# Optimization experiments

Measured on AMD Instinct MI355X. Metric: run time of the kernel, lower is better.

The kernel has to match this reference:

```python
import jax, jax.numpy as jnp
import numpy as np

B, S, H, I, L, NH = 1, 256, 384, 1536, 2, 8

def _gelu(x):
    return jax.nn.gelu(x, approximate=False)  # torch nn.GELU default = exact erf

def _ln(x, g, b, eps=1e-5):
    m = x.mean(-1, keepdims=True)
    v = jnp.var(x, axis=-1, keepdims=True)
    return (x - m) / jnp.sqrt(v + eps) * g + b

def _mha(x, Wqkv, bqkv, Wo, bo):
    b_, s_, h_ = x.shape
    d = h_ // NH
    qkv = x @ Wqkv.T + bqkv  # [B,S,3H]
    q, k, v = jnp.split(qkv, 3, axis=-1)
    sp = lambda t: t.reshape(b_, s_, NH, d).transpose(0, 2, 1, 3)  # [B,NH,S,d]
    q, k, v = sp(q), sp(k), sp(v)
    att = jax.nn.softmax(jnp.einsum('bhqd,bhkd->bhqk', q * (1.0 / np.sqrt(d)), k), axis=-1)
    o = jnp.einsum('bhqk,bhkd->bhqd', att, v).transpose(0, 2, 1, 3).reshape(b_, s_, h_)
    return o @ Wo.T + bo

def _forward(hidden_states, Wqkv, bqkv, Wo, bo, W1, b1, W2, b2, g1, be1, g2, be2,
             Wbil, bbil, Wc1, bc1, Wc2, bc2, Wih, bih, Whh, bhh, Wp1, bp1, Wp2, bp2,
             Wout, bout, reasoning_steps):
    x = hidden_states
    rstate = jnp.zeros((x.shape[0], x.shape[-1]), x.dtype)
    cprobs, conts = [], []
    for _ in range(reasoning_steps):
        # symbolic reasoning layers (eval mode: dropout off)
        for l in range(L):
            x = _ln(x + _mha(x, Wqkv[l], bqkv[l], Wo[l], bo[l]), g1[l], be1[l])
            ff = _gelu(x @ W1[l].T + b1[l]) @ W2[l].T + b2[l]
            x = _ln(x + ff, g2[l], be2[l])
        # contradiction detector: bilinear over all token pairs
        tmp = jnp.einsum('bix,oxy->bioy', x, Wbil)            # [B,S,H,H]
        inter = jnp.einsum('bioy,bjy->bijo', tmp, x) + bbil   # [B,S,S,H]
        h1 = _gelu(inter @ Wc1.T + bc1)                       # [B,S,S,H]
        logits = jnp.einsum('bijh,h->bij', h1, Wc2[0]) + bc2[0]
        cprobs.append(jax.nn.sigmoid(logits))
        # recursive reasoning controller (GRUCell on mean-pooled states)
        pooled = x.mean(axis=1)
        gi = pooled @ Wih.T + bih
        gh = rstate @ Whh.T + bhh
        ir, iz, inn = jnp.split(gi, 3, axis=-1)
        hr, hz, hn = jnp.split(gh, 3, axis=-1)
        r = jax.nn.sigmoid(ir + hr)
        z = jax.nn.sigmoid(iz + hz)
        n = jnp.tanh(inn + r * hn)
        rstate = (1.0 - z) * n + z * rstate
        conts.append(jax.nn.sigmoid(_gelu(rstate @ Wp1.T + bp1) @ Wp2[0] + bp2[0]))
    final = x @ Wout.T + bout
    return final, jnp.stack(cprobs), jnp.stack(conts)

def setup_inputs():
    key = jax.random.key(0)
    ks = iter(jax.random.split(key, 40))
    rn = lambda shape, s=0.02: jax.random.normal(next(ks), shape, jnp.float32) * s
    return {
        'hidden_states': jax.random.normal(next(ks), (B, S, H), jnp.float32),
        'Wqkv': rn((L, 3 * H, H)), 'bqkv': jnp.zeros((L, 3 * H)),
        'Wo': rn((L, H, H)), 'bo': jnp.zeros((L, H)),
        'W1': rn((L, I, H)), 'b1': jnp.zeros((L, I)),
        'W2': rn((L, H, I)), 'b2': jnp.zeros((L, H)),
        'g1': jnp.ones((L, H)), 'be1': jnp.zeros((L, H)),
        'g2': jnp.ones((L, H)), 'be2': jnp.zeros((L, H)),
        'Wbil': rn((H, H, H)), 'bbil': jnp.zeros((H,)),
        'Wc1': rn((H, H)), 'bc1': jnp.zeros((H,)),
        'Wc2': rn((1, H)), 'bc2': jnp.zeros((1,)),
        'Wih': rn((3 * H, H)), 'bih': jnp.zeros((3 * H,)),
        'Whh': rn((3 * H, H)), 'bhh': jnp.zeros((3 * H,)),
        'Wp1': rn((H, H)), 'bp1': jnp.zeros((H,)),
        'Wp2': rn((1, H)), 'bp2': jnp.zeros((1,)),
        'Wout': rn((H, H)), 'bout': jnp.zeros((H,)),
        'reasoning_steps': 2,
    }

def reference(hidden_states, Wqkv, bqkv, Wo, bo, W1, b1, W2, b2, g1, be1, g2, be2,
              Wbil, bbil, Wc1, bc1, Wc2, bc2, Wih, bih, Whh, bhh, Wp1, bp1, Wp2, bp2,
              Wout, bout, reasoning_steps):
    return _forward(hidden_states, Wqkv, bqkv, Wo, bo, W1, b1, W2, b2, g1, be1, g2, be2,
                    Wbil, bbil, Wc1, bc1, Wc2, bc2, Wih, bih, Whh, bhh, Wp1, bp1, Wp2, bp2,
                    Wout, bout, reasoning_steps)
```

## Files before the change

### kernel.cpp

```cpp
#include <hip/hip_runtime.h>

typedef __attribute__((ext_vector_type(4))) float f32x4;
typedef __attribute__((ext_vector_type(8))) short s16x8;

#define DEVI __device__ __forceinline__

DEVI float b2f(short s) {
  union { float f; unsigned u; } v; v.u = ((unsigned)(unsigned short)s) << 16; return v.f;
}
DEVI short f2b(float f) {
  union { float f; unsigned u; } v; v.f = f;
  unsigned u = v.u;
  u += 0x7FFFu + ((u >> 16) & 1u);
  return (short)(u >> 16);
}
DEVI float gelu_f(float x) {
  float z2 = 1.5957691216f * x * (1.0f + 0.044715f * x * x);
  float e = __expf(z2);
  float th = 1.0f - 2.0f / (e + 1.0f);
  return 0.5f * x * (1.0f + th);
}
DEVI float sigm_f(float x) { return 1.0f / (1.0f + expf(-x)); }

DEVI void gld16(const short* g, const short* l) {
  __builtin_amdgcn_global_load_lds((const __attribute__((address_space(1))) void*)g,
                                   (__attribute__((address_space(3))) void*)l, 16, 0, 0);
}

template<bool BIAS, bool GELU_ACT, bool OUT_BF16>
__global__ __launch_bounds__(256)
void gemm_fast_k(const short* __restrict__ A, const short* __restrict__ B,
                 const float* __restrict__ bias, void* __restrict__ Cv,
                 int M, int N, int K,
                 long long sA, long long sB, long long sC)
{
  __shared__ short As[128 * 64];
  __shared__ short Bs[128 * 64];
  const int bz = blockIdx.z;
  const int n0 = blockIdx.x * 128;
  const int m0 = blockIdx.y * 128;
  const int t = threadIdx.x, lane = t & 63, wave = t >> 6;
  const int wm = wave >> 1, wn = wave & 1;
  const short* Ab = A + bz * sA;
  const short* Bb = B + bz * sB;
  const int srow = lane >> 3;
  const int scol = ((lane & 7) ^ srow) * 8;
  const int fr = lane & 15, fs = lane >> 4;

  f32x4 acc[4][4];
#pragma unroll
  for (int i = 0; i < 4; ++i)
#pragma unroll
    for (int j = 0; j < 4; ++j) acc[i][j] = f32x4{0.f, 0.f, 0.f, 0.f};

  for (int k0 = 0; k0 < K; k0 += 64) {
#pragma unroll
    for (int q = 0; q < 4; ++q) {
      int c = wave * 4 + q;
      gld16(Ab + (long long)(m0 + c * 8 + srow) * K + k0 + scol, &As[c * 512]);
      gld16(Bb + (long long)(n0 + c * 8 + srow) * K + k0 + scol, &Bs[c * 512]);
    }
    __syncthreads();
    s16x8 af[4][2], bfv[4][2];
#pragma unroll
    for (int i = 0; i < 4; ++i) {
      int row = wm * 64 + i * 16 + fr;
#pragma unroll
      for (int s = 0; s < 2; ++s)
        af[i][s] = *(const s16x8*)&As[row * 64 + (((s * 4 + fs) ^ (fr & 7)) * 8)];
    }
#pragma unroll
    for (int j = 0; j < 4; ++j) {
      int row = wn * 64 + j * 16 + fr;
#pragma unroll
      for (int s = 0; s < 2; ++s)
        bfv[j][s] = *(const s16x8*)&Bs[row * 64 + (((s * 4 + fs) ^ (fr & 7)) * 8)];
    }
#pragma unroll
    for (int s = 0; s < 2; ++s)
#pragma unroll
      for (int i = 0; i < 4; ++i)
#pragma unroll
        for (int j = 0; j < 4; ++j)
          acc[i][j] = __builtin_amdgcn_mfma_f32_16x16x32_bf16(af[i][s], bfv[j][s], acc[i][j], 0, 0, 0);
    __syncthreads();
  }

#pragma unroll
  for (int i = 0; i < 4; ++i) {
    int rowb = m0 + wm * 64 + i * 16 + fs * 4;
#pragma unroll
    for (int j = 0; j < 4; ++j) {
      int col = n0 + wn * 64 + j * 16 + fr;
      float bb = BIAS ? bias[col] : 0.0f;
#pragma unroll
      for (int u = 0; u < 4; ++u) {
        float v = acc[i][j][u] + bb;
        if constexpr (GELU_ACT) v = gelu_f(v);
        long long off = bz * sC + (long long)(rowb + u) * N + col;
        if constexpr (OUT_BF16) ((short*)Cv)[off] = f2b(v);
        else                    ((float*)Cv)[off] = v;
      }
    }
  }
}

template<bool BIAS, bool GELU_ACT, bool OUT_BF16>
__global__ __launch_bounds__(256)
void gemm64_k(const short* __restrict__ A, const short* __restrict__ B,
              const float* __restrict__ bias, void* __restrict__ Cv,
              int M, int N, int K)
{
  __shared__ short As[64 * 32];
  __shared__ short Bs[64 * 32];
  const int n0 = blockIdx.x * 64;
  const int m0 = blockIdx.y * 64;
  const int t = threadIdx.x, lane = t & 63, wave = t >> 6;
  const int wm = wave >> 1, wn = wave & 1;
  const int srow = lane >> 2;
  const int scol = (lane & 3) * 8;
  const int fr = lane & 15, fs = lane >> 4;

  f32x4 acc[2][2];
#pragma unroll
  for (int i = 0; i < 2; ++i)
#pragma unroll
    for (int j = 0; j < 2; ++j) acc[i][j] = f32x4{0.f, 0.f, 0.f, 0.f};

  for (int k0 = 0; k0 < K; k0 += 32) {
    gld16(A + (long long)(m0 + wave * 16 + srow) * K + k0 + scol, &As[wave * 512]);
    gld16(B + (long long)(n0 + wave * 16 + srow) * K + k0 + scol, &Bs[wave * 512]);
    __syncthreads();
    s16x8 af[2], bfv[2];
#pragma unroll
    for (int i = 0; i < 2; ++i) af[i]  = *(const s16x8*)&As[(wm * 32 + i * 16 + fr) * 32 + fs * 8];
#pragma unroll
    for (int j = 0; j < 2; ++j) bfv[j] = *(const s16x8*)&Bs[(wn * 32 + j * 16 + fr) * 32 + fs * 8];
#pragma unroll
    for (int i = 0; i < 2; ++i)
#pragma unroll
      for (int j = 0; j < 2; ++j)
        acc[i][j] = __builtin_amdgcn_mfma_f32_16x16x32_bf16(af[i], bfv[j], acc[i][j], 0, 0, 0);
    __syncthreads();
  }

#pragma unroll
  for (int i = 0; i < 2; ++i) {
    int rowb = m0 + wm * 32 + i * 16 + fs * 4;
#pragma unroll
    for (int j = 0; j < 2; ++j) {
      int col = n0 + wn * 32 + j * 16 + fr;
      float bb = BIAS ? bias[col] : 0.0f;
#pragma unroll
      for (int u = 0; u < 4; ++u) {
        float v = acc[i][j][u] + bb;
        if constexpr (GELU_ACT) v = gelu_f(v);
        long long off = (long long)(rowb + u) * N + col;
        if constexpr (OUT_BF16) ((short*)Cv)[off] = f2b(v);
        else                    ((float*)Cv)[off] = v;
      }
    }
  }
}

__global__ __launch_bounds__(256)
void transpose_k(const float* __restrict__ W, short* __restrict__ WT)
{
  __shared__ short L[64 * 68];
  const int o  = blockIdx.z;
  const int x0 = blockIdx.x * 64, y0 = blockIdx.y * 64;
  const float* Wo = W  + (long long)o * 147456;
  short*      WTo = WT + (long long)o * 147456;
  const int t  = threadIdx.x;
  const int rr = t >> 4;
  const int cc = (t & 15) * 4;
#pragma unroll
  for (int q = 0; q < 4; ++q) {
    int xl = rr + 16 * q;
    float4 v = *(const float4*)(Wo + (x0 + xl) * 384 + y0 + cc);
    short4 p; p.x = f2b(v.x); p.y = f2b(v.y); p.z = f2b(v.z); p.w = f2b(v.w);
    *(short4*)&L[xl * 68 + cc] = p;
  }
  __syncthreads();
#pragma unroll
  for (int q = 0; q < 4; ++q) {
    int yl = rr + 16 * q;
    short4 p;
    p.x = L[(cc + 0) * 68 + yl];
    p.y = L[(cc + 1) * 68 + yl];
    p.z = L[(cc + 2) * 68 + yl];
    p.w = L[(cc + 3) * 68 + yl];
    *(short4*)(WTo + (y0 + yl) * 384 + x0 + cc) = p;
  }
}

__global__ __launch_bounds__(256)
void convw_k(const float* __restrict__ W, short* __restrict__ Wb, int n)
{
  int i = (blockIdx.x * 256 + threadIdx.x) * 4;
  if (i < n) {
    float4 v = *(const float4*)(W + i);
    short4 p; p.x = f2b(v.x); p.y = f2b(v.y); p.z = f2b(v.z); p.w = f2b(v.w);
    *(short4*)(Wb + i) = p;
  }
}

__global__ __launch_bounds__(256)
void attn_k(const float* __restrict__ qkv, short* __restrict__ outb)
{
  __shared__ short Ks[256 * 48];
  __shared__ short Vs[256 * 48];
  __shared__ float Ps[32][258];
  const int h  = blockIdx.y;
  const int q0 = blockIdx.x * 32;
  const int t = threadIdx.x, lane = t & 63, wave = t >> 6;
  for (int idx = t; idx < 256 * 48; idx += 256) {
    int j = idx / 48, d = idx - j * 48;
    Ks[idx] = f2b(qkv[j * 1152 + 384 + h * 48 + d]);
    Vs[idx] = f2b(qkv[j * 1152 + 768 + h * 48 + d]);
  }
  __syncthreads();
  const int part = lane & 7;
  const int rl   = wave * 8 + (lane >> 3);
  const int row  = q0 + rl;
  float q[48];
#pragma unroll
  for (int d = 0; d < 48; ++d) q[d] = qkv[row * 1152 + h * 48 + d] * 0.14433756729740644f;
  float mx = -1e30f;
  for (int jj = 0; jj < 32; ++jj) {
    int j = jj * 8 + part;
    float a = 0.f;
#pragma unroll
    for (int dd = 0; dd < 12; ++dd) {
      short4 kk = *(const short4*)&Ks[j * 48 + dd * 4];
      a += q[dd*4+0]*b2f(kk.x) + q[dd*4+1]*b2f(kk.y) + q[dd*4+2]*b2f(kk.z) + q[dd*4+3]*b2f(kk.w);
    }
    Ps[rl][j] = a;
    mx = fmaxf(mx, a);
  }
  mx = fmaxf(mx, __shfl_xor(mx, 1));
  mx = fmaxf(mx, __shfl_xor(mx, 2));
  mx = fmaxf(mx, __shfl_xor(mx, 4));
  float sum = 0.f;
  for (int jj = 0; jj < 32; ++jj) {
    int j = jj * 8 + part;
    float e = expf(Ps[rl][j] - mx);
    Ps[rl][j] = e;
    sum += e;
  }
  sum += __shfl_xor(sum, 1); sum += __shfl_xor(sum, 2); sum += __shfl_xor(sum, 4);
  const float inv = 1.f / sum;
  __syncthreads();
  float o[6] = {0.f, 0.f, 0.f, 0.f, 0.f, 0.f};
  const int vb = part * 6;
  for (int j = 0; j < 256; ++j) {
    float p = Ps[rl][j];
    int base = j * 48 + vb;
#pragma unroll
    for (int dd = 0; dd < 3; ++dd) {
      short2 vv = *(const short2*)&Vs[base + dd * 2];
      o[dd*2]   += p * b2f(vv.x);
      o[dd*2+1] += p * b2f(vv.y);
    }
  }
#pragma unroll
  for (int d = 0; d < 6; ++d) outb[row * 384 + h * 48 + vb + d] = f2b(o[d] * inv);
}

__global__ __launch_bounds__(128)
void ln_k(const float* __restrict__ x, const float* __restrict__ d,
          const float* __restrict__ g, const float* __restrict__ b,
          float* __restrict__ xo, short* __restrict__ xob)
{
  const int row = blockIdx.x, t = threadIdx.x;
  float v[3]; float s = 0.f, ss = 0.f;
#pragma unroll
  for (int i = 0; i < 3; ++i) {
    int c = t + 128 * i;
    float u = x[row * 384 + c] + d[row * 384 + c];
    v[i] = u; s += u; ss += u * u;
  }
#pragma unroll
  for (int m = 1; m < 64; m <<= 1) { s += __shfl_xor(s, m); ss += __shfl_xor(ss, m); }
  __shared__ float sh[4];
  if ((t & 63) == 0) { sh[(t >> 6) * 2] = s; sh[(t >> 6) * 2 + 1] = ss; }
  __syncthreads();
  s = sh[0] + sh[2]; ss = sh[1] + sh[3];
  float mean = s * (1.f / 384.f);
  float var  = ss * (1.f / 384.f) - mean * mean;
  float rstd = rsqrtf(var + 1e-5f);
#pragma unroll
  for (int i = 0; i < 3; ++i) {
    int c = t + 128 * i;
    float y = (v[i] - mean) * rstd * g[c] + b[c];
    xo[row * 384 + c]  = y;
    xob[row * 384 + c] = f2b(y);
  }
}

__global__ void init_k(const float* __restrict__ hs, float* __restrict__ x,
                       short* __restrict__ xb, float* __restrict__ rstate)
{
  int i = blockIdx.x * 256 + threadIdx.x;
  if (i < 98304) { float v = hs[i]; x[i] = v; xb[i] = f2b(v); }
  if (i < 384) rstate[i] = 0.f;
}

__global__ __launch_bounds__(256)
void logits_k(const short* __restrict__ h1, const float* __restrict__ Wc2,
              const float* __restrict__ bc2, float* __restrict__ outp)
{
  const int t = threadIdx.x, lane = t & 63, wave = t >> 6;
  const int row = blockIdx.x * 4 + wave;
  const short* hr = h1 + (long long)row * 384;
  float a = 0.f;
#pragma unroll
  for (int e = 0; e < 6; ++e) { int c = lane + 64 * e; a += b2f(hr[c]) * Wc2[c]; }
#pragma unroll
  for (int m = 1; m < 64; m <<= 1) a += __shfl_xor(a, m);
  if (lane == 0) outp[row] = sigm_f(a + bc2[0]);
}

__global__ __launch_bounds__(384)
void pool1_k(const float* __restrict__ x, float* __restrict__ partial)
{
  const int t = threadIdx.x, p = blockIdx.x;
  float s = 0.f;
  const float* xr = x + p * 32 * 384;
#pragma unroll 4
  for (int i = 0; i < 32; ++i) s += xr[i * 384 + t];
  partial[p * 384 + t] = s;
}

__global__ __launch_bounds__(256)
void gih_k(const float* __restrict__ Wih, const float* __restrict__ bih,
           const float* __restrict__ Whh, const float* __restrict__ bhh,
           const float* __restrict__ partial, const float* __restrict__ rstate,
           float* __restrict__ gi, float* __restrict__ gh)
{
  const int t = threadIdx.x, lane = t & 63, wave = t >> 6;
  const int r = blockIdx.x * 4 + wave;
  float a = 0.f, b = 0.f;
#pragma unroll
  for (int e = 0; e < 6; ++e) {
    int c = lane + 64 * e;
    float pc = 0.f;
#pragma unroll
    for (int p = 0; p < 8; ++p) pc += partial[p * 384 + c];
    pc *= (1.f / 256.f);
    a += Wih[r * 384 + c] * pc;
    b += Whh[r * 384 + c] * rstate[c];
  }
#pragma unroll
  for (int m = 1; m < 64; m <<= 1) { a += __shfl_xor(a, m); b += __shfl_xor(b, m); }
  if (lane == 0) { gi[r] = a + bih[r]; gh[r] = b + bhh[r]; }
}

__global__ __launch_bounds__(384)
void gru2_k(const float* __restrict__ gi, const float* __restrict__ gh,
            float* __restrict__ rstate, float* __restrict__ hnew)
{
  const int t = threadIdx.x;
  float r = sigm_f(gi[t] + gh[t]);
  float z = sigm_f(gi[384 + t] + gh[384 + t]);
  float n = tanhf(gi[768 + t] + r * gh[768 + t]);
  float h = (1.f - z) * n + z * rstate[t];
  rstate[t] = h;
  hnew[t] = h;
}

__global__ __launch_bounds__(256)
void p1_k(const float* __restrict__ Wp1, const float* __restrict__ bp1,
          const float* __restrict__ hnew, float* __restrict__ p1)
{
  const int t = threadIdx.x, lane = t & 63, wave = t >> 6;
  const int r = blockIdx.x * 4 + wave;
  float a = 0.f;
#pragma unroll
  for (int e = 0; e < 6; ++e) { int c = lane + 64 * e; a += Wp1[r * 384 + c] * hnew[c]; }
#pragma unroll
  for (int m = 1; m < 64; m <<= 1) a += __shfl_xor(a, m);
  if (lane == 0) p1[r] = gelu_f(a + bp1[r]);
}

__global__ __launch_bounds__(64)
void cont_k(const float* __restrict__ p1, const float* __restrict__ Wp2,
            const float* __restrict__ bp2, float* __restrict__ out_cont)
{
  const int lane = threadIdx.x;
  float a = 0.f;
#pragma unroll
  for (int e = 0; e < 6; ++e) { int c = lane + 64 * e; a += p1[c] * Wp2[c]; }
#pragma unroll
  for (int m = 1; m < 64; m <<= 1) a += __shfl_xor(a, m);
  if (lane == 0) out_cont[0] = sigm_f(a + bp2[0]);
}

extern "C" void kernel_launch(void* const* d_in, const int* in_sizes, int n_in,
                              void* d_out, int out_size, void* d_ws, size_t ws_size,
                              hipStream_t stream)
{
  const float* hs   = (const float*)d_in[0];
  const float* Wqkv = (const float*)d_in[1];
  const float* bqkv = (const float*)d_in[2];
  const float* Wo   = (const float*)d_in[3];
  const float* bo   = (const float*)d_in[4];
  const float* W1   = (const float*)d_in[5];
  const float* b1   = (const float*)d_in[6];
  const float* W2   = (const float*)d_in[7];
  const float* b2   = (const float*)d_in[8];
  const float* g1   = (const float*)d_in[9];
  const float* be1  = (const float*)d_in[10];
  const float* g2   = (const float*)d_in[11];
  const float* be2  = (const float*)d_in[12];
  const float* Wbil = (const float*)d_in[13];
  const float* bbil = (const float*)d_in[14];
  const float* Wc1  = (const float*)d_in[15];
  const float* bc1  = (const float*)d_in[16];
  const float* Wc2  = (const float*)d_in[17];
  const float* bc2  = (const float*)d_in[18];
  const float* Wih  = (const float*)d_in[19];
  const float* bih  = (const float*)d_in[20];
  const float* Whh  = (const float*)d_in[21];
  const float* bhh  = (const float*)d_in[22];
  const float* Wp1  = (const float*)d_in[23];
  const float* bp1  = (const float*)d_in[24];
  const float* Wp2  = (const float*)d_in[25];
  const float* bp2  = (const float*)d_in[26];
  const float* Wout = (const float*)d_in[27];
  const float* bout = (const float*)d_in[28];
  float* out = (float*)d_out;

  char* ws = (char*)d_ws;
  size_t off = 0;
  auto alloc = [&](size_t bytes) -> char* {
    char* p = ws + off; off += (bytes + 255) & ~(size_t)255; return p;
  };
  short* wbilT   = (short*)alloc(56623104ULL * 2);
  short* tmp     = (short*)alloc(256ULL * 147456 * 2);
  short* inter   = (short*)alloc(256ULL * 98304 * 2);
  float* x       = (float*)alloc(98304 * 4);
  short* xb      = (short*)alloc(98304 * 2);
  float* qkv     = (float*)alloc(294912 * 4);
  short* attnb   = (short*)alloc(98304 * 2);
  float* delta   = (float*)alloc(98304 * 4);
  short* ff1b    = (short*)alloc(393216 * 2);
  float* rstate  = (float*)alloc(384 * 4);
  float* partial = (float*)alloc(8 * 384 * 4);
  float* gi      = (float*)alloc(1152 * 4);
  float* gh      = (float*)alloc(1152 * 4);
  float* hnew    = (float*)alloc(384 * 4);
  float* p1buf   = (float*)alloc(384 * 4);
  short* wc1b    = (short*)alloc(147456 * 2);
  short* wqkvb   = (short*)alloc(884736ULL * 2);
  short* wob     = (short*)alloc(294912ULL * 2);
  short* w1b     = (short*)alloc(1179648ULL * 2);
  short* w2b     = (short*)alloc(1179648ULL * 2);
  short* woutb   = (short*)alloc(147456 * 2);
  short* h1 = tmp;
  (void)ws_size; (void)in_sizes; (void)n_in; (void)out_size;

  dim3 B256(256);

  init_k<<<dim3(384), B256, 0, stream>>>(hs, x, xb, rstate);
  transpose_k<<<dim3(6, 6, 384), B256, 0, stream>>>(Wbil, wbilT);
  convw_k<<<dim3(144),  B256, 0, stream>>>(Wc1, wc1b, 147456);
  convw_k<<<dim3(864),  B256, 0, stream>>>(Wqkv, wqkvb, 884736);
  convw_k<<<dim3(288),  B256, 0, stream>>>(Wo, wob, 294912);
  convw_k<<<dim3(1152), B256, 0, stream>>>(W1, w1b, 1179648);
  convw_k<<<dim3(1152), B256, 0, stream>>>(W2, w2b, 1179648);
  convw_k<<<dim3(144),  B256, 0, stream>>>(Wout, woutb, 147456);

  for (int s = 0; s < 2; ++s) {
    for (int l = 0; l < 2; ++l) {
      gemm64_k<true, false, false><<<dim3(18, 4), B256, 0, stream>>>(
          xb, wqkvb + l * 442368, bqkv + l * 1152, qkv, 256, 1152, 384);
      attn_k<<<dim3(8, 8), B256, 0, stream>>>(qkv, attnb);
      gemm64_k<true, false, false><<<dim3(6, 4), B256, 0, stream>>>(
          attnb, wob + l * 147456, bo + l * 384, delta, 256, 384, 384);
      ln_k<<<dim3(256), dim3(128), 0, stream>>>(x, delta, g1 + l * 384, be1 + l * 384, x, xb);
      gemm64_k<true, true, true><<<dim3(24, 4), B256, 0, stream>>>(
          xb, w1b + l * 589824, b1 + l * 1536, ff1b, 256, 1536, 384);
      gemm64_k<true, false, false><<<dim3(6, 4), B256, 0, stream>>>(
          ff1b, w2b + l * 589824, b2 + l * 384, delta, 256, 384, 1536);
      ln_k<<<dim3(256), dim3(128), 0, stream>>>(x, delta, g2 + l * 384, be2 + l * 384, x, xb);
    }
    gemm_fast_k<false, false, true><<<dim3(1152, 2, 1), B256, 0, stream>>>(
        xb, wbilT, (const float*)nullptr, tmp, 256, 147456, 384, 0, 0, 0);
    gemm_fast_k<true, false, true><<<dim3(3, 2, 256), B256, 0, stream>>>(
        xb, tmp, bbil, inter, 256, 384, 384, 0, 147456LL, 98304LL);
    gemm_fast_k<true, true, true><<<dim3(3, 2, 256), B256, 0, stream>>>(
        inter, wc1b, bc1, h1, 256, 384, 384, 98304LL, 0, 98304LL);
    logits_k<<<dim3(16384), B256, 0, stream>>>(h1, Wc2, bc2, out + 98304 + s * 65536);
    pool1_k<<<dim3(8), dim3(384), 0, stream>>>(x, partial);
    gih_k<<<dim3(288), B256, 0, stream>>>(Wih, bih, Whh, bhh, partial, rstate, gi, gh);
    gru2_k<<<dim3(1), dim3(384), 0, stream>>>(gi, gh, rstate, hnew);
    p1_k<<<dim3(96), B256, 0, stream>>>(Wp1, bp1, hnew, p1buf);
    cont_k<<<dim3(1), dim3(64), 0, stream>>>(p1buf, Wp2, bp2, out + 98304 + 131072 + s);
  }
  gemm64_k<true, false, false><<<dim3(6, 4), B256, 0, stream>>>(
      xb, woutb, bout, out, 256, 384, 384);
}
```

Before: 698.6 us.

## Double-buffer LDS tiles in both GEMM kernels to overlap loads with MFMA

Both GEMM kernels now use two LDS buffers and issue the global-to-LDS load for the next K tile before computing on the current one, dropping one barrier per iteration. In the large kernel the K step also shrinks from 64 to 32 and the XOR swizzle is removed, so LDS stays the same size. The goal is to hide global load latency behind matrix math. The risks are more LDS bank conflicts without the swizzle and twice as many loop iterations. There is also a correctness concern: the asynchronous global_load_lds into the next buffer is only covered by a single barrier, so whether it has completed before use depends on how the compiler places the vmcnt wait.

```diff
diff --git a/kernel.cpp b/kernel.cpp
--- a/kernel.cpp
+++ b/kernel.cpp
@@ -34,8 +34,8 @@
                  int M, int N, int K,
                  long long sA, long long sB, long long sC)
 {
-  __shared__ short As[128 * 64];
-  __shared__ short Bs[128 * 64];
+  __shared__ short As[2][128 * 32];
+  __shared__ short Bs[2][128 * 32];
   const int bz = blockIdx.z;
   const int n0 = blockIdx.x * 128;
   const int m0 = blockIdx.y * 128;
@@ -43,8 +43,8 @@
   const int wm = wave >> 1, wn = wave & 1;
   const short* Ab = A + bz * sA;
   const short* Bb = B + bz * sB;
-  const int srow = lane >> 3;
-  const int scol = ((lane & 7) ^ srow) * 8;
+  const int srow = lane >> 2;
+  const int scol = (lane & 3) * 8;
   const int fr = lane & 15, fs = lane >> 4;
 
   f32x4 acc[4][4];
@@ -53,37 +53,32 @@
 #pragma unroll
     for (int j = 0; j < 4; ++j) acc[i][j] = f32x4{0.f, 0.f, 0.f, 0.f};
 
-  for (int k0 = 0; k0 < K; k0 += 64) {
-#pragma unroll
-    for (int q = 0; q < 4; ++q) {
-      int c = wave * 4 + q;
-      gld16(Ab + (long long)(m0 + c * 8 + srow) * K + k0 + scol, &As[c * 512]);
-      gld16(Bb + (long long)(n0 + c * 8 + srow) * K + k0 + scol, &Bs[c * 512]);
+  auto stage = [&](int b, int k0) {
+#pragma unroll
+    for (int q = 0; q < 2; ++q) {
+      int c = wave * 2 + q;
+      gld16(Ab + (long long)(m0 + c * 16 + srow) * K + k0 + scol, &As[b][c * 512]);
+      gld16(Bb + (long long)(n0 + c * 16 + srow) * K + k0 + scol, &Bs[b][c * 512]);
     }
-    __syncthreads();
-    s16x8 af[4][2], bfv[4][2];
-#pragma unroll
-    for (int i = 0; i < 4; ++i) {
-      int row = wm * 64 + i * 16 + fr;
-#pragma unroll
-      for (int s = 0; s < 2; ++s)
-        af[i][s] = *(const s16x8*)&As[row * 64 + (((s * 4 + fs) ^ (fr & 7)) * 8)];
-    }
-#pragma unroll
-    for (int j = 0; j < 4; ++j) {
-      int row = wn * 64 + j * 16 + fr;
-#pragma unroll
-      for (int s = 0; s < 2; ++s)
-        bfv[j][s] = *(const s16x8*)&Bs[row * 64 + (((s * 4 + fs) ^ (fr & 7)) * 8)];
-    }
-#pragma unroll
-    for (int s = 0; s < 2; ++s)
-#pragma unroll
-      for (int i = 0; i < 4; ++i)
-#pragma unroll
-        for (int j = 0; j < 4; ++j)
-          acc[i][j] = __builtin_amdgcn_mfma_f32_16x16x32_bf16(af[i][s], bfv[j][s], acc[i][j], 0, 0, 0);
-    __syncthreads();
+  };
+
+  const int NT = K >> 5;
+  stage(0, 0);
+  __syncthreads();
+  for (int tt = 0; tt < NT; ++tt) {
+    const int cur = tt & 1;
+    if (tt + 1 < NT) stage(cur ^ 1, (tt + 1) << 5);
+    s16x8 af[4], bfv[4];
+#pragma unroll
+    for (int i = 0; i < 4; ++i) af[i]  = *(const s16x8*)&As[cur][(wm * 64 + i * 16 + fr) * 32 + fs * 8];
+#pragma unroll
+    for (int j = 0; j < 4; ++j) bfv[j] = *(const s16x8*)&Bs[cur][(wn * 64 + j * 16 + fr) * 32 + fs * 8];
+#pragma unroll
+    for (int i = 0; i < 4; ++i)
+#pragma unroll
+      for (int j = 0; j < 4; ++j)
+        acc[i][j] = __builtin_amdgcn_mfma_f32_16x16x32_bf16(af[i], bfv[j], acc[i][j], 0, 0, 0);
+    if (tt + 1 < NT) __syncthreads();
   }
 
 #pragma unroll
@@ -111,8 +106,8 @@
               const float* __restrict__ bias, void* __restrict__ Cv,
               int M, int N, int K)
 {
-  __shared__ short As[64 * 32];
-  __shared__ short Bs[64 * 32];
+  __shared__ short As[2][64 * 32];
+  __shared__ short Bs[2][64 * 32];
   const int n0 = blockIdx.x * 64;
   const int m0 = blockIdx.y * 64;
   const int t = threadIdx.x, lane = t & 63, wave = t >> 6;
@@ -127,21 +122,28 @@
 #pragma unroll
     for (int j = 0; j < 2; ++j) acc[i][j] = f32x4{0.f, 0.f, 0.f, 0.f};
 
-  for (int k0 = 0; k0 < K; k0 += 32) {
-    gld16(A + (long long)(m0 + wave * 16 + srow) * K + k0 + scol, &As[wave * 512]);
-    gld16(B + (long long)(n0 + wave * 16 + srow) * K + k0 + scol, &Bs[wave * 512]);
-    __syncthreads();
+  auto stage = [&](int b, int k0) {
+    gld16(A + (long long)(m0 + wave * 16 + srow) * K + k0 + scol, &As[b][wave * 512]);
+    gld16(B + (long long)(n0 + wave * 16 + srow) * K + k0 + scol, &Bs[b][wave * 512]);
+  };
+
+  const int NT = K >> 5;
+  stage(0, 0);
+  __syncthreads();
+  for (int tt = 0; tt < NT; ++tt) {
+    const int cur = tt & 1;
+    if (tt + 1 < NT) stage(cur ^ 1, (tt + 1) << 5);
     s16x8 af[2], bfv[2];
 #pragma unroll
-    for (int i = 0; i < 2; ++i) af[i]  = *(const s16x8*)&As[(wm * 32 + i * 16 + fr) * 32 + fs * 8];
-#pragma unroll
-    for (int j = 0; j < 2; ++j) bfv[j] = *(const s16x8*)&Bs[(wn * 32 + j * 16 + fr) * 32 + fs * 8];
+    for (int i = 0; i < 2; ++i) af[i]  = *(const s16x8*)&As[cur][(wm * 32 + i * 16 + fr) * 32 + fs * 8];
+#pragma unroll
+    for (int j = 0; j < 2; ++j) bfv[j] = *(const s16x8*)&Bs[cur][(wn * 32 + j * 16 + fr) * 32 + fs * 8];
 #pragma unroll
     for (int i = 0; i < 2; ++i)
 #pragma unroll
       for (int j = 0; j < 2; ++j)
         acc[i][j] = __builtin_amdgcn_mfma_f32_16x16x32_bf16(af[i], bfv[j], acc[i][j], 0, 0, 0);
-    __syncthreads();
+    if (tt + 1 < NT) __syncthreads();
   }
 
 #pragma unroll
```

New measurement: 693.7 us. No clear change (-0.7%).
